# Performance work log

Measured on AMD Instinct MI355X. Metric: run time of the kernel, lower is better.

The kernel has to match this reference:

```python
import jax, jax.numpy as jnp
import numpy as np

B, C, H, W = 16, 256, 48, 160
BASELINE = 0.54
REL_ELEV = 1.65
H_MEAN = 1.535


def setup_inputs() -> dict:
    key = jax.random.key(0)
    k = jax.random.split(key, 5)
    features = jax.random.normal(k[0], (B, C, H, W), dtype=jnp.float32)
    # realistic KITTI-style P2 (full-resolution intrinsics; forward divides rows 0:2 by 16)
    base = np.zeros((3, 4), np.float32)
    base[0, 0] = 721.5; base[1, 1] = 721.5
    base[0, 2] = 609.5; base[1, 2] = 172.8
    base[2, 2] = 1.0;   base[1, 3] = 0.2
    P2 = jnp.asarray(base)[None] + 0.5 * jax.random.uniform(k[1], (B, 3, 4), dtype=jnp.float32)
    w_disp = 0.05 * jax.random.normal(k[2], (1, C, 3, 3), dtype=jnp.float32)  # disp_create conv3x3
    b_disp = jnp.zeros((1,), jnp.float32)
    w_ext = 0.05 * jax.random.normal(k[3], (C, C + 1), dtype=jnp.float32)     # extract conv1x1 (O,I)
    b_ext = jnp.zeros((C,), jnp.float32)
    alpha = 0.5 * jnp.ones((1,), jnp.float32)  # nn.Parameter (init 0.0; nonzero to exercise path)
    return {"features": features, "P2": P2, "w_disp": w_disp, "b_disp": b_disp,
            "w_ext": w_ext, "b_ext": b_ext, "alpha": alpha}


def _grid_sample_border(feat, gx, gy):
    """Bilinear grid_sample, padding_mode='border', align_corners=True.
    feat: (B,C1,H,W); gx, gy: (B,H,W) in [-1,1]."""
    Bs, C1, Hs, Ws = feat.shape
    ix = jnp.clip((gx + 1.0) * 0.5 * (Ws - 1), 0.0, Ws - 1)
    iy = jnp.clip((gy + 1.0) * 0.5 * (Hs - 1), 0.0, Hs - 1)
    ix0 = jnp.floor(ix); iy0 = jnp.floor(iy)
    ix1 = jnp.minimum(ix0 + 1.0, Ws - 1); iy1 = jnp.minimum(iy0 + 1.0, Hs - 1)
    wx = (ix - ix0).reshape(Bs, 1, -1)
    wy = (iy - iy0).reshape(Bs, 1, -1)
    flat = feat.reshape(Bs, C1, Hs * Ws)

    def gather(f, yq, xq):
        idx = (yq * Ws + xq).astype(jnp.int32).reshape(-1)
        return f[:, idx]  # (C1, H*W)

    g = jax.vmap(gather)
    v00 = g(flat, iy0, ix0); v01 = g(flat, iy0, ix1)
    v10 = g(flat, iy1, ix0); v11 = g(flat, iy1, ix1)
    out = (v00 * (1 - wx) * (1 - wy) + v01 * wx * (1 - wy)
           + v10 * (1 - wx) * wy + v11 * wx * wy)
    return out.reshape(Bs, C1, Hs, Ws)


def reference(features, P2, w_disp, b_disp, w_ext, b_ext, alpha):
    x = features
    Bs = x.shape[0]
    P2 = P2.at[:, 0:2].set(P2[:, 0:2] / 16.0)
    # disp_create: conv3x3 -> tanh, then detach-scaled
    d = jax.lax.conv_general_dilated(x, w_disp, (1, 1), 'SAME',
                                     dimension_numbers=('NCHW', 'OIHW', 'NCHW'))
    d = jnp.tanh(d + b_disp[None, :, None, None])
    disp = 0.1 * (0.05 * d + 0.95 * jax.lax.stop_gradient(d))  # (B,1,H,W)

    yy = jnp.arange(H, dtype=jnp.float32)[None, :, None]  # (1,H,1): row index
    fy = P2[:, 1:2, 1:2]; cy = P2[:, 1:2, 2:3]; Ty = P2[:, 1:2, 3:4]  # (B,1,1)
    disparity = jax.nn.relu(fy * BASELINE * (yy - cy)
                            / (jnp.abs(fy * REL_ELEV + Ty) + 1e-10))  # (B,H,1)
    disparity = jnp.broadcast_to(disparity, (Bs, H, W))

    x_base = jnp.broadcast_to(jnp.linspace(-1.0, 1.0, W, dtype=jnp.float32)[None, None, :], (Bs, H, W))
    y_base = jnp.linspace(-1.0, 1.0, H, dtype=jnp.float32)[None, :, None]  # (1,H,1)
    y_shifts_base = jax.nn.relu(H_MEAN * (yy - cy) / (2.0 * (REL_ELEV - 0.5 * H_MEAN))) / (H * 0.5)
    y_shifts = y_shifts_base + disp[:, 0]  # (B,H,W)
    gy = y_base + y_shifts

    feats = jnp.concatenate([disparity[:, None], x], axis=1)  # (B,C+1,H,W)
    samp = _grid_sample_border(feats, x_base, gy)
    out = jnp.einsum('oc,bchw->bohw', w_ext, samp) + b_ext[None, :, None, None]
    return jax.nn.relu(x + out * alpha[0])
```

## Files before the change

kernel.cpp:

```cpp
#include <hip/hip_runtime.h>
#include <stdint.h>

#define NB 16
#define NC 256
#define NH 48
#define NW 160
#define HW (NH*NW)
#define NP (NB*HW)

static __device__ __forceinline__ unsigned short f2bf(float f){
  union { float f; uint32_t u; } v; v.f = f;
  uint32_t u = v.u;
  uint32_t r = (u + 0x7FFFu + ((u >> 16) & 1u)) >> 16;
  return (unsigned short)r;
}
static __device__ __forceinline__ float bf2f(unsigned short h){
  union { float f; uint32_t u; } v; v.u = ((uint32_t)h) << 16; return v.f;
}

__global__ __launch_bounds__(256) void kw_conv(const float* __restrict__ w_ext,
                                               const float* __restrict__ w_disp,
                                               unsigned short* __restrict__ Wb,
                                               unsigned short* __restrict__ Wtap){
  if (blockIdx.x < 256){
    int idx = blockIdx.x * 256 + threadIdx.x;
    int o = idx >> 8, c = idx & 255;
    Wb[idx] = f2bf(w_ext[o * 257 + 1 + c]);
  } else {
    int c = threadIdx.x;
    #pragma unroll
    for (int m = 0; m < 16; ++m){
      float v = (m < 9) ? w_disp[c * 9 + m] : 0.f;
      Wtap[m * 256 + c] = f2bf(v);
    }
  }
}

typedef __attribute__((ext_vector_type(8))) short bf16x8;
typedef __attribute__((ext_vector_type(4))) float f32x4;

__global__ __launch_bounds__(256) void kb_gemm(
    const float* __restrict__ x,
    const unsigned short* __restrict__ Wb,
    const unsigned short* __restrict__ Wtap,
    unsigned short* __restrict__ U,
    float* __restrict__ T)
{
  __shared__ __align__(16) unsigned short smem[4 * 512];
  int bx = blockIdx.x;
  int b  = bx / 120;
  int nt = bx - b * 120;
  int p0 = nt * 64;

  int tid  = threadIdx.x;
  int lane = tid & 63;
  int w    = tid >> 6;
  int l15 = lane & 15;
  int lq  = lane >> 4;

  int sn  = tid & 63;
  int skq = tid >> 6;
  const float* xbase = x + ((size_t)b * NC) * HW + p0 + sn;
  unsigned short* swr = smem + (sn >> 4) * 512 + ((sn & 15) + skq * 16) * 8;

  f32x4 zero = {0.f, 0.f, 0.f, 0.f};
  f32x4 acc[4][4];
  f32x4 acct[4];
  #pragma unroll
  for (int mi = 0; mi < 4; ++mi){
    acct[mi] = zero;
    #pragma unroll
    for (int ni = 0; ni < 4; ++ni) acc[mi][ni] = zero;
  }

  for (int ks = 0; ks < 8; ++ks){
    __syncthreads();
    {
      int c0 = ks * 32 + skq * 8;
      const float* src = xbase + (size_t)c0 * HW;
      unsigned short h[8];
      #pragma unroll
      for (int j = 0; j < 8; ++j)
        h[j] = f2bf(src[(size_t)j * HW]);
      *(bf16x8*)swr = *(bf16x8*)h;
    }
    __syncthreads();

    bf16x8 af[4], bg[4];
    #pragma unroll
    for (int mi = 0; mi < 4; ++mi){
      int m = w * 64 + mi * 16 + l15;
      af[mi] = *(const bf16x8*)(Wb + (size_t)m * 256 + ks * 32 + lq * 8);
    }
    #pragma unroll
    for (int ni = 0; ni < 4; ++ni)
      bg[ni] = *(const bf16x8*)(smem + ni * 512 + lane * 8);

    #pragma unroll
    for (int mi = 0; mi < 4; ++mi)
      #pragma unroll
      for (int ni = 0; ni < 4; ++ni)
        acc[mi][ni] = __builtin_amdgcn_mfma_f32_16x16x32_bf16(af[mi], bg[ni], acc[mi][ni], 0, 0, 0);

    if (w == 0){
      bf16x8 at = *(const bf16x8*)(Wtap + (size_t)l15 * 256 + ks * 32 + lq * 8);
      #pragma unroll
      for (int ni = 0; ni < 4; ++ni)
        acct[ni] = __builtin_amdgcn_mfma_f32_16x16x32_bf16(at, bg[ni], acct[ni], 0, 0, 0);
    }
  }

  #pragma unroll
  for (int mi = 0; mi < 4; ++mi){
    #pragma unroll
    for (int ni = 0; ni < 4; ++ni){
      int o = w * 64 + mi * 16 + lq * 4;
      int n = ni * 16 + l15;
      size_t base = ((size_t)(b * NC + o)) * HW + p0 + n;
      #pragma unroll
      for (int r = 0; r < 4; ++r)
        U[base + (size_t)r * HW] = f2bf(acc[mi][ni][r]);
    }
  }
  if (w == 0){
    #pragma unroll
    for (int ni = 0; ni < 4; ++ni){
      int n = ni * 16 + l15;
      #pragma unroll
      for (int r = 0; r < 4; ++r){
        int k = lq * 4 + r;
        if (k < 9)
          T[(size_t)k * NP + (size_t)b * HW + p0 + n] = acct[ni][r];
      }
    }
  }
}

__global__ __launch_bounds__(256) void kp_grid(
    const float* __restrict__ P2, const float* __restrict__ b_disp,
    const float* __restrict__ T, float4* __restrict__ pre)
{
  int p = blockIdx.x * 256 + threadIdx.x;
  int b  = p / HW;
  int hw = p - b * HW;
  int y  = hw / NW;
  int xx = hw - y * NW;

  float d = 0.f;
  #pragma unroll
  for (int ky = 0; ky < 3; ++ky){
    int yy2 = y + ky - 1;
    if (yy2 < 0 || yy2 >= NH) continue;
    #pragma unroll
    for (int kx = 0; kx < 3; ++kx){
      int xx2 = xx + kx - 1;
      if (xx2 < 0 || xx2 >= NW) continue;
      d += T[(size_t)(ky * 3 + kx) * NP + b * HW + yy2 * NW + xx2];
    }
  }
  float th = tanhf(d + b_disp[0]);

  float fy = P2[b * 12 + 5] * 0.0625f;
  float cy = P2[b * 12 + 6] * 0.0625f;
  float Ty = P2[b * 12 + 7] * 0.0625f;

  float ysb   = fmaxf(1.535f * ((float)y - cy) / 1.765f, 0.f) * (1.f / 24.f);
  float ybase = -1.f + (float)y * (2.f / 47.f);
  float gy = ybase + ysb + 0.1f * th;
  float iy = fminf(fmaxf((gy + 1.f) * 0.5f * 47.f, 0.f), 47.f);
  float fiy0 = floorf(iy);
  float wy = iy - fiy0;
  int iy0 = (int)fiy0;
  int iy1 = min(iy0 + 1, 47);

  float inv_den = 1.f / (fabsf(fy * 1.65f + Ty) + 1e-10f);
  float dr0 = fmaxf(fy * 0.54f * ((float)iy0 - cy) * inv_den, 0.f);
  float dr1 = fmaxf(fy * 0.54f * ((float)iy1 - cy) * inv_den, 0.f);
  float dlerp = (1.f - wy) * dr0 + wy * dr1;

  float4 pr;
  pr.x = wy; pr.y = dlerp;
  pr.z = __int_as_float(iy0 * NW + xx);
  pr.w = __int_as_float(iy1 * NW + xx);
  pre[p] = pr;
}

__global__ __launch_bounds__(256) void kc_epilogue(
    const float* __restrict__ x, const float* __restrict__ w_ext,
    const float* __restrict__ b_ext, const float* __restrict__ alpha,
    const unsigned short* __restrict__ U, const float4* __restrict__ pre,
    float* __restrict__ out)
{
  int bx = blockIdx.x;
  int ptile = bx >> 3;
  int cg    = bx & 7;
  int p = ptile * 256 + threadIdx.x;
  int b  = p / HW;
  int hw = p - b * HW;

  float4 pr = pre[p];
  float wy    = pr.x;
  float dlerp = pr.y;
  int off0 = __float_as_int(pr.z);
  int off1 = __float_as_int(pr.w);
  float w1 = 1.f - wy;
  float al = alpha[0];

  size_t base0 = (size_t)(b * NC) * HW;
  const unsigned short* Ub = U + base0;
  const float* xb = x + base0 + hw;
  float* ob = out + base0 + hw;

  int o0 = cg * 32;
  #pragma unroll 4
  for (int o = o0; o < o0 + 32; ++o){
    float u0 = bf2f(Ub[(size_t)o * HW + off0]);
    float u1 = bf2f(Ub[(size_t)o * HW + off1]);
    float val = w1 * u0 + wy * u1 + w_ext[o * 257] * dlerp + b_ext[o];
    float r = xb[(size_t)o * HW] + al * val;
    ob[(size_t)o * HW] = fmaxf(r, 0.f);
  }
}

extern "C" void kernel_launch(void* const* d_in, const int* in_sizes, int n_in,
                              void* d_out, int out_size, void* d_ws, size_t ws_size,
                              hipStream_t stream) {
  const float* features = (const float*)d_in[0];
  const float* P2       = (const float*)d_in[1];
  const float* w_disp   = (const float*)d_in[2];
  const float* b_disp   = (const float*)d_in[3];
  const float* w_ext    = (const float*)d_in[4];
  const float* b_ext    = (const float*)d_in[5];
  const float* alpha    = (const float*)d_in[6];
  float* out = (float*)d_out;

  char* ws = (char*)d_ws;
  const size_t U_bytes   = (size_t)NP * 256 * 2;
  const size_t T_bytes   = (size_t)9 * NP * 4;
  const size_t pre_bytes = (size_t)NP * 16;
  unsigned short* U    = (unsigned short*)ws;
  float*          T    = (float*)(ws + U_bytes);
  float4*         pre  = (float4*)(ws + U_bytes + T_bytes);
  unsigned short* Wb   = (unsigned short*)(ws + U_bytes + T_bytes + pre_bytes);
  unsigned short* Wtap = Wb + 256 * 256;

  hipLaunchKernelGGL(kw_conv,     dim3(257),  dim3(256), 0, stream, w_ext, w_disp, Wb, Wtap);
  hipLaunchKernelGGL(kb_gemm,     dim3(1920), dim3(256), 0, stream, features, Wb, Wtap, U, T);
  hipLaunchKernelGGL(kp_grid,     dim3(480),  dim3(256), 0, stream, P2, b_disp, T, pre);
  hipLaunchKernelGGL(kc_epilogue, dim3(3840), dim3(256), 0, stream,
                     features, w_ext, b_ext, alpha, U, pre, out);
}
```

Before: 321.5 us.

## Pre-transpose features to bf16 pixel-major buffer so GEMM loads B directly

Result: slower. 387.2 us (+20.4%).

```diff
diff --git a/kernel.cpp b/kernel.cpp
--- a/kernel.cpp
+++ b/kernel.cpp
@@ -17,6 +17,9 @@
 static __device__ __forceinline__ float bf2f(unsigned short h){
   union { float f; uint32_t u; } v; v.u = ((uint32_t)h) << 16; return v.f;
 }
+
+typedef __attribute__((ext_vector_type(8))) short bf16x8;
+typedef __attribute__((ext_vector_type(4))) float f32x4;
 
 __global__ __launch_bounds__(256) void kw_conv(const float* __restrict__ w_ext,
                                                const float* __restrict__ w_disp,
@@ -36,17 +39,35 @@
   }
 }
 
-typedef __attribute__((ext_vector_type(8))) short bf16x8;
-typedef __attribute__((ext_vector_type(4))) float f32x4;
+__global__ __launch_bounds__(256) void kt_stage(const float* __restrict__ x,
+                                                unsigned short* __restrict__ xT){
+  int p0 = blockIdx.x * 64;
+  int b  = p0 / HW;
+  int hw0 = p0 - b * HW;
+  int t  = threadIdx.x;
+  int sn  = t & 63;
+  int skq = t >> 6;
+  const float* xbase = x + ((size_t)(b * NC)) * HW + hw0 + sn;
+
+  #pragma unroll
+  for (int it = 0; it < 8; ++it){
+    int c0 = it * 32 + skq * 8;
+    const float* src = xbase + (size_t)c0 * HW;
+    unsigned short h[8];
+    #pragma unroll
+    for (int j = 0; j < 8; ++j)
+      h[j] = f2bf(src[(size_t)j * HW]);
+    *(bf16x8*)(xT + ((size_t)(p0 + sn)) * 256 + c0) = *(bf16x8*)h;
+  }
+}
 
 __global__ __launch_bounds__(256) void kb_gemm(
-    const float* __restrict__ x,
     const unsigned short* __restrict__ Wb,
+    const unsigned short* __restrict__ xT,
     const unsigned short* __restrict__ Wtap,
     unsigned short* __restrict__ U,
     float* __restrict__ T)
 {
-  __shared__ __align__(16) unsigned short smem[4 * 512];
   int bx = blockIdx.x;
   int b  = bx / 120;
   int nt = bx - b * 120;
@@ -58,10 +79,9 @@
   int l15 = lane & 15;
   int lq  = lane >> 4;
 
-  int sn  = tid & 63;
-  int skq = tid >> 6;
-  const float* xbase = x + ((size_t)b * NC) * HW + p0 + sn;
-  unsigned short* swr = smem + (sn >> 4) * 512 + ((sn & 15) + skq * 16) * 8;
+  const unsigned short* Abase = Wb   + ((size_t)(w * 64 + l15) * 256) + lq * 8;
+  const unsigned short* Bbase = xT   + ((size_t)(b * HW + p0 + l15) * 256) + lq * 8;
+  const unsigned short* Tbase = Wtap + ((size_t)l15 * 256) + lq * 8;
 
   f32x4 zero = {0.f, 0.f, 0.f, 0.f};
   f32x4 acc[4][4];
@@ -74,27 +94,13 @@
   }
 
   for (int ks = 0; ks < 8; ++ks){
-    __syncthreads();
-    {
-      int c0 = ks * 32 + skq * 8;
-      const float* src = xbase + (size_t)c0 * HW;
-      unsigned short h[8];
-      #pragma unroll
-      for (int j = 0; j < 8; ++j)
-        h[j] = f2bf(src[(size_t)j * HW]);
-      *(bf16x8*)swr = *(bf16x8*)h;
-    }
-    __syncthreads();
-
     bf16x8 af[4], bg[4];
     #pragma unroll
-    for (int mi = 0; mi < 4; ++mi){
-      int m = w * 64 + mi * 16 + l15;
-      af[mi] = *(const bf16x8*)(Wb + (size_t)m * 256 + ks * 32 + lq * 8);
-    }
+    for (int mi = 0; mi < 4; ++mi)
+      af[mi] = *(const bf16x8*)(Abase + (size_t)(mi * 16) * 256 + ks * 32);
     #pragma unroll
     for (int ni = 0; ni < 4; ++ni)
-      bg[ni] = *(const bf16x8*)(smem + ni * 512 + lane * 8);
+      bg[ni] = *(const bf16x8*)(Bbase + (size_t)(ni * 16) * 256 + ks * 32);
 
     #pragma unroll
     for (int mi = 0; mi < 4; ++mi)
@@ -103,7 +109,7 @@
         acc[mi][ni] = __builtin_amdgcn_mfma_f32_16x16x32_bf16(af[mi], bg[ni], acc[mi][ni], 0, 0, 0);
 
     if (w == 0){
-      bf16x8 at = *(const bf16x8*)(Wtap + (size_t)l15 * 256 + ks * 32 + lq * 8);
+      bf16x8 at = *(const bf16x8*)(Tbase + ks * 32);
       #pragma unroll
       for (int ni = 0; ni < 4; ++ni)
         acct[ni] = __builtin_amdgcn_mfma_f32_16x16x32_bf16(at, bg[ni], acct[ni], 0, 0, 0);
@@ -235,17 +241,19 @@
   float* out = (float*)d_out;
 
   char* ws = (char*)d_ws;
-  const size_t U_bytes   = (size_t)NP * 256 * 2;
-  const size_t T_bytes   = (size_t)9 * NP * 4;
-  const size_t pre_bytes = (size_t)NP * 16;
-  unsigned short* U    = (unsigned short*)ws;
-  float*          T    = (float*)(ws + U_bytes);
-  float4*         pre  = (float4*)(ws + U_bytes + T_bytes);
-  unsigned short* Wb   = (unsigned short*)(ws + U_bytes + T_bytes + pre_bytes);
+  const size_t xT_bytes = (size_t)NP * 256 * 2;
+  const size_t U_bytes  = (size_t)NP * 256 * 2;
+  const size_t T_bytes  = (size_t)9 * NP * 4;
+  unsigned short* xT   = (unsigned short*)ws;
+  unsigned short* U    = (unsigned short*)(ws + xT_bytes);
+  float*          T    = (float*)(ws + xT_bytes + U_bytes);
+  unsigned short* Wb   = (unsigned short*)(ws + xT_bytes + U_bytes + T_bytes);
   unsigned short* Wtap = Wb + 256 * 256;
+  float4*         pre  = (float4*)ws;
 
   hipLaunchKernelGGL(kw_conv,     dim3(257),  dim3(256), 0, stream, w_ext, w_disp, Wb, Wtap);
-  hipLaunchKernelGGL(kb_gemm,     dim3(1920), dim3(256), 0, stream, features, Wb, Wtap, U, T);
+  hipLaunchKernelGGL(kt_stage,    dim3(1920), dim3(256), 0, stream, features, xT);
+  hipLaunchKernelGGL(kb_gemm,     dim3(1920), dim3(256), 0, stream, Wb, xT, Wtap, U, T);
   hipLaunchKernelGGL(kp_grid,     dim3(480),  dim3(256), 0, stream, P2, b_disp, T, pre);
   hipLaunchKernelGGL(kc_epilogue, dim3(3840), dim3(256), 0, stream,
                      features, w_ext, b_ext, alpha, U, pre, out);
```
